# Kernel tuning notes

Hardware: AMD Instinct MI355X
Metric: run time of the kernel (lower is better)

Reference implementation:

```python
import jax, jax.numpy as jnp
import numpy as np

B, H, W = 8, 64, 64
DIM, NH, WS = 384, 6, 14
HD = DIM // NH
MLP = int(DIM * 4.0)
EPS = 1e-5
SCALE = HD ** -0.5


def setup_inputs() -> dict:
    key = jax.random.key(0)
    ks = jax.random.split(key, 8)
    init = lambda k, shape: (jax.random.normal(k, shape, dtype=jnp.float32) * 0.02)
    return {
        "x": jax.random.normal(ks[0], (B, H, W, DIM), dtype=jnp.float32),
        "ln1_w": jnp.ones((DIM,), jnp.float32),
        "ln1_b": jnp.zeros((DIM,), jnp.float32),
        "qkv_w": init(ks[1], (DIM, 3 * DIM)),
        "qkv_b": jnp.zeros((3 * DIM,), jnp.float32),
        "proj_w": init(ks[2], (DIM, DIM)),
        "proj_b": jnp.zeros((DIM,), jnp.float32),
        "rel_pos_h": init(ks[3], (2 * WS - 1, HD)),
        "rel_pos_w": init(ks[4], (2 * WS - 1, HD)),
        "ln2_w": jnp.ones((DIM,), jnp.float32),
        "ln2_b": jnp.zeros((DIM,), jnp.float32),
        "fc1_w": init(ks[5], (DIM, MLP)),
        "fc1_b": jnp.zeros((MLP,), jnp.float32),
        "fc2_w": init(ks[6], (MLP, DIM)),
        "fc2_b": jnp.zeros((DIM,), jnp.float32),
    }


def _layernorm(x, w, b):
    m = x.mean(-1, keepdims=True)
    v = ((x - m) ** 2).mean(-1, keepdims=True)
    return (x - m) * jax.lax.rsqrt(v + EPS) * w + b


def _get_rel_pos(rel_pos, ws):
    # q_size == k_size == ws and rel_pos has 2*ws-1 rows, so torch's
    # F.interpolate to max_rel_dist=2*ws-1 is an identity; direct indexing.
    coords = jnp.arange(ws)[:, None] - jnp.arange(ws)[None, :] + (ws - 1)
    return rel_pos[coords]  # (ws, ws, head_dim)


def _attention(xw, qkv_w, qkv_b, proj_w, proj_b, rel_pos_h, rel_pos_w):
    Bw = xw.shape[0]
    N = WS * WS
    qkv = xw.reshape(Bw, N, DIM) @ qkv_w + qkv_b  # (Bw, N, 3*DIM)
    qkv = qkv.reshape(Bw, N, 3, NH, HD).transpose(2, 0, 3, 1, 4).reshape(3, Bw * NH, N, HD)
    q, k, v = qkv[0], qkv[1], qkv[2]
    attn = jnp.einsum("bqd,bkd->bqk", q * SCALE, k)  # (Bw*NH, N, N)
    Rh = _get_rel_pos(rel_pos_h, WS)
    Rw = _get_rel_pos(rel_pos_w, WS)
    rq = q.reshape(Bw * NH, WS, WS, HD)
    rel_h = jnp.einsum("bhwc,hkc->bhwk", rq, Rh)
    rel_w = jnp.einsum("bhwc,wkc->bhwk", rq, Rw)
    attn = (attn.reshape(Bw * NH, WS, WS, WS, WS)
            + rel_h[:, :, :, :, None]
            + rel_w[:, :, :, None, :]).reshape(Bw * NH, N, N)
    attn = jax.nn.softmax(attn, axis=-1)
    out = jnp.einsum("bqk,bkd->bqd", attn, v)
    out = out.reshape(Bw, NH, WS, WS, HD).transpose(0, 2, 3, 1, 4).reshape(Bw, WS, WS, DIM)
    return out @ proj_w + proj_b


def reference(x, ln1_w, ln1_b, qkv_w, qkv_b, proj_w, proj_b, rel_pos_h, rel_pos_w,
              ln2_w, ln2_b, fc1_w, fc1_b, fc2_w, fc2_b):
    shortcut = x
    h = _layernorm(x, ln1_w, ln1_b)
    pad_h = (WS - H % WS) % WS
    pad_w = (WS - W % WS) % WS
    Hp, Wp = H + pad_h, W + pad_w
    hp = jnp.pad(h, ((0, 0), (0, pad_h), (0, pad_w), (0, 0)))
    # window partition: (B, Hp, Wp, C) -> (B*nWin, WS, WS, C)
    wins = hp.reshape(B, Hp // WS, WS, Wp // WS, WS, DIM)
    wins = wins.transpose(0, 1, 3, 2, 4, 5).reshape(-1, WS, WS, DIM)
    wins = _attention(wins, qkv_w, qkv_b, proj_w, proj_b, rel_pos_h, rel_pos_w)
    # window unpartition
    y = wins.reshape(B, Hp // WS, Wp // WS, WS, WS, DIM)
    y = y.transpose(0, 1, 3, 2, 4, 5).reshape(B, Hp, Wp, DIM)[:, :H, :W, :]
    x = shortcut + y
    h2 = _layernorm(x, ln2_w, ln2_b)
    mlp = jax.nn.gelu(h2 @ fc1_w + fc1_b, approximate=False) @ fc2_w + fc2_b
    return x + mlp
```

## Files before the change

### kernel.cpp

```cpp
#include <hip/hip_runtime.h>
#include <math.h>

#define DIMC 384
#define NHD  6
#define HD   64
#define WSZ  14
#define NTOK 196
#define NWIN 200
#define NWH  1200
#define MWIN 39200
#define MX   32768
#define MLPD 1536

typedef short short8 __attribute__((ext_vector_type(8)));
typedef float f32x4 __attribute__((ext_vector_type(4)));
typedef float f32x16 __attribute__((ext_vector_type(16)));

__device__ __forceinline__ unsigned short f2bf(float f) {
  unsigned int u = __float_as_uint(f);
  u = (u + 0x7fffu + ((u >> 16) & 1u)) >> 16;
  return (unsigned short)u;
}
__device__ __forceinline__ unsigned int pkbf(float a, float b) {
  unsigned int r; asm("v_cvt_pk_bf16_f32 %0, %1, %2" : "=v"(r) : "v"(a), "v"(b)); return r;
}
__device__ __forceinline__ float gelu_t(float x) {
  float z = 1.5957691216057308f * (x + 0.044715f * x * x * x);
  float e = __expf(z);
  float th = 1.f - 2.f * __builtin_amdgcn_rcpf(e + 1.f);
  return 0.5f * x * (1.f + th);
}

typedef const __attribute__((address_space(1))) unsigned int* gptr_t;
typedef __attribute__((address_space(3))) unsigned int* lptr_t;
__device__ __forceinline__ void gload16(const unsigned short* g, unsigned short* l) {
  __builtin_amdgcn_global_load_lds((gptr_t)(const void*)g, (lptr_t)(void*)l, 16, 0, 0);
}

__global__ void wtrans_kernel(const float* __restrict__ in, unsigned short* __restrict__ out,
                              int K, int N) {
  int id = blockIdx.x * 256 + threadIdx.x;
  if (id >= K * N) return;
  int n = id / K, k = id - n * K;
  out[id] = f2bf(in[(size_t)k * N + n]);
}

__global__ void relprep_kernel(const float* __restrict__ relh, const float* __restrict__ relw,
                               unsigned short* __restrict__ relcat) {
  int id = blockIdx.x * 256 + threadIdx.x;
  if (id >= 64 * 64) return;
  int rc = id >> 6, d = id & 63;
  float v = 0.f;
  if (rc < 27) v = relh[rc * 64 + d] * 8.f;
  else if (rc < 54) v = relw[(rc - 27) * 64 + d] * 8.f;
  relcat[id] = f2bf(v);
}

__global__ void vpad_kernel(unsigned short* __restrict__ vT) {
  int id = blockIdx.x * 256 + threadIdx.x;
  if (id >= 76800 * 3) return;
  int row = id / 3, part = id - row * 3;
  *(int2*)(vT + (size_t)row * 208 + 196 + part * 4) = make_int2(0, 0);
}

__global__ __launch_bounds__(64) void ln1win_kernel(const float* __restrict__ x,
    const float* __restrict__ w, const float* __restrict__ b, unsigned short* __restrict__ xw) {
  int t = blockIdx.x;
  int lane = threadIdx.x;
  int win = t / NTOK, p = t - win * NTOK;
  int bb = win / 25, rem = win - bb * 25;
  int wi = rem / 5, wj = rem - wi * 5;
  int i = p / WSZ, j = p - i * WSZ;
  int r = wi * WSZ + i, c = wj * WSZ + j;
  unsigned short* o = xw + (size_t)t * DIMC;
  if (r >= 64 || c >= 64) {
    #pragma unroll
    for (int q = 0; q < 6; q++) o[lane + q * 64] = 0;
    return;
  }
  const float* xr = x + (((size_t)bb * 64 + r) * 64 + c) * DIMC;
  float v[6]; float s = 0.f, s2 = 0.f;
  #pragma unroll
  for (int q = 0; q < 6; q++) { float f = xr[lane + q * 64]; v[q] = f; s += f; s2 += f * f; }
  #pragma unroll
  for (int off = 32; off; off >>= 1) { s += __shfl_xor(s, off); s2 += __shfl_xor(s2, off); }
  float mean = s * (1.f / DIMC);
  float var  = s2 * (1.f / DIMC) - mean * mean;
  float rstd = rsqrtf(var + 1e-5f);
  #pragma unroll
  for (int q = 0; q < 6; q++) {
    int d = lane + q * 64;
    o[d] = f2bf((v[q] - mean) * rstd * w[d] + b[d]);
  }
}

__global__ __launch_bounds__(64) void ln2_kernel(const float* __restrict__ x2,
    const float* __restrict__ w, const float* __restrict__ b, unsigned short* __restrict__ h2) {
  int t = blockIdx.x; int lane = threadIdx.x;
  const float* xr = x2 + (size_t)t * DIMC;
  unsigned short* o = h2 + (size_t)t * DIMC;
  float v[6]; float s = 0.f, s2 = 0.f;
  #pragma unroll
  for (int q = 0; q < 6; q++) { float f = xr[lane + q * 64]; v[q] = f; s += f; s2 += f * f; }
  #pragma unroll
  for (int off = 32; off; off >>= 1) { s += __shfl_xor(s, off); s2 += __shfl_xor(s2, off); }
  float mean = s * (1.f / DIMC);
  float var  = s2 * (1.f / DIMC) - mean * mean;
  float rstd = rsqrtf(var + 1e-5f);
  #pragma unroll
  for (int q = 0; q < 6; q++) {
    int d = lane + q * 64;
    o[d] = f2bf((v[q] - mean) * rstd * w[d] + b[d]);
  }
}

template <int EPI>
__global__ __launch_bounds__(256) void gemm_kernel(
    const unsigned short* __restrict__ A, const unsigned short* __restrict__ WT,
    int Mrows, int Kd,
    const float* __restrict__ bias, const float* __restrict__ addin,
    float* __restrict__ outf, unsigned short* __restrict__ outb,
    unsigned short* __restrict__ outb2) {
  __shared__ unsigned short As[3][128 * 32];
  __shared__ unsigned short Bs[3][128 * 32];
  const int nwg = gridDim.x * gridDim.y;
  const int flat = blockIdx.y * gridDim.x + blockIdx.x;
  const int xcd = flat & 7, q_ = nwg >> 3, r_ = nwg & 7;
  const int wg = (xcd < r_ ? xcd * (q_ + 1) : r_ * (q_ + 1) + (xcd - r_) * q_) + (flat >> 3);
  const int bx = wg / gridDim.y, by = wg - bx * gridDim.y;
  const int row0 = bx * 128, col0 = by * 128;
  const int tid = threadIdx.x;
  const int l = tid & 63, wid = tid >> 6;
  const int fr = l & 15, fk = (l >> 4) * 8;
  const int wr = (wid >> 1) * 64, wc = (wid & 1) * 64;
  const int sr = l >> 2, sc = (l & 3) * 8;
  const int scs = sc ^ (((sr >> 1) & 3) << 3);
  const int rsw = ((fr >> 1) & 3) << 3;
  f32x4 acc[4][4] = {};
  const unsigned short* ap = A + (size_t)row0 * Kd;
  const unsigned short* bp = WT + (size_t)col0 * Kd;
  const int nt = Kd >> 5;

  auto stage = [&](int t, int b) {
    const int k0 = t * 32;
    #pragma unroll
    for (int j = 0; j < 2; j++) {
      int chunk = j * 4 + wid;
      gload16(ap + (size_t)(chunk * 16 + sr) * Kd + k0 + scs, &As[b][chunk * 512]);
      gload16(bp + (size_t)(chunk * 16 + sr) * Kd + k0 + scs, &Bs[b][chunk * 512]);
    }
  };
  stage(0, 0);
  stage(1, 1);
  int c = 0;
  for (int t = 0; t < nt; ++t) {
    if (t < nt - 1) asm volatile("s_waitcnt vmcnt(4)" ::: "memory");
    else            asm volatile("s_waitcnt vmcnt(0)" ::: "memory");
    __builtin_amdgcn_s_barrier();
    __builtin_amdgcn_sched_barrier(0);
    if (t + 2 < nt) stage(t + 2, (c + 2 >= 3) ? c - 1 : c + 2);
    short8 a[4], b[4];
    #pragma unroll
    for (int fi = 0; fi < 4; fi++) {
      a[fi] = *(const short8*)&As[c][(wr + fi * 16 + fr) * 32 + (fk ^ rsw)];
      b[fi] = *(const short8*)&Bs[c][(wc + fi * 16 + fr) * 32 + (fk ^ rsw)];
    }
    asm volatile("s_waitcnt lgkmcnt(0)" ::: "memory");
    __builtin_amdgcn_sched_barrier(0);
    __builtin_amdgcn_s_setprio(1);
    #pragma unroll
    for (int fi = 0; fi < 4; fi++)
      #pragma unroll
      for (int fj = 0; fj < 4; fj++)
        acc[fi][fj] = __builtin_amdgcn_mfma_f32_16x16x32_bf16(b[fj], a[fi], acc[fi][fj], 0, 0, 0);
    __builtin_amdgcn_s_setprio(0);
    c = (c + 1 >= 3) ? 0 : c + 1;
  }
  #pragma unroll
  for (int fi = 0; fi < 4; fi++) {
    const int gr = row0 + wr + fi * 16 + fr;
    if (gr >= Mrows) continue;
    int wv_ = 0, p = 0, valid = 1; size_t pixbase = 0;
    if (EPI == 0 || EPI == 1) { wv_ = gr / NTOK; p = gr - wv_ * NTOK; }
    if (EPI == 1) {
      int bb = wv_ / 25, rem2 = wv_ - bb * 25;
      int wi = rem2 / 5, wj = rem2 - wi * 5;
      int i = p / WSZ, j = p - i * WSZ;
      int rr = wi * WSZ + i, cc = wj * WSZ + j;
      valid = (rr < 64) && (cc < 64);
      pixbase = (((size_t)bb * 64 + rr) * 64 + cc) * DIMC;
    }
    #pragma unroll
    for (int fj = 0; fj < 4; fj++) {
      const int gcb = col0 + wc + fj * 16 + (l >> 4) * 4;
      f32x4 v = acc[fi][fj];
      float4 bv = *(const float4*)&bias[gcb];
      float t0 = v[0] + bv.x, t1 = v[1] + bv.y, t2 = v[2] + bv.z, t3 = v[3] + bv.w;
      if (EPI == 0) {
        int s = gcb / 384, rem = gcb - s * 384;
        int hh = rem >> 6, d0 = gcb & 63;
        int whh = wv_ * NHD + hh;
        if (s == 0) { t0 *= 0.125f; t1 *= 0.125f; t2 *= 0.125f; t3 *= 0.125f; }
        if (s < 2) {
          *(int2*)&outb[((size_t)s * NWH + whh) * (NTOK * 64) + p * 64 + d0] =
              make_int2((int)pkbf(t0, t1), (int)pkbf(t2, t3));
        } else {
          unsigned short* vb = outb2 + ((size_t)whh * 64 + d0) * 208 + p;
          vb[0] = f2bf(t0); vb[208] = f2bf(t1); vb[416] = f2bf(t2); vb[624] = f2bf(t3);
        }
      } else if (EPI == 1) {
        if (valid) {
          size_t idx = pixbase + gcb;
          float4 ad = *(const float4*)&addin[idx];
          *(float4*)&outf[idx] = make_float4(t0 + ad.x, t1 + ad.y, t2 + ad.z, t3 + ad.w);
        }
      } else if (EPI == 2) {
        *(int2*)&outb[(size_t)gr * MLPD + gcb] =
            make_int2((int)pkbf(gelu_t(t0), gelu_t(t1)), (int)pkbf(gelu_t(t2), gelu_t(t3)));
      } else {
        size_t idx = (size_t)gr * DIMC + gcb;
        float4 ad = *(const float4*)&addin[idx];
        *(float4*)&outf[idx] = make_float4(t0 + ad.x, t1 + ad.y, t2 + ad.z, t3 + ad.w);
      }
    }
  }
}

template <bool TAIL>
__device__ __forceinline__ void attn_chunk(
    int kk, int l31, int hi,
    const unsigned short* __restrict__ kg,
    const unsigned short* __restrict__ VT,
    const short8* qf, const short8* qrel,
    f32x16& olo, f32x16& ohi_, float& m_reg, float& s_run) {
  int key = kk * 32 + l31;
  int keyc = (TAIL && key > 195) ? 195 : key;
  f32x16 S = {};
  __builtin_amdgcn_s_setprio(1);
  #pragma unroll
  for (int m = 0; m < 4; m++) {
    short8 kf = *(const short8*)(kg + (size_t)keyc * 64 + m * 16 + hi * 8);
    S = __builtin_amdgcn_mfma_f32_32x32x16_bf16(kf, qf[m], S, 0, 0, 0);
  }
  {
    int ki = keyc / 14, kj = keyc - ki * 14;
    #pragma unroll
    for (int m2 = 0; m2 < 2; m2++) {
      short8 kh;
      #pragma unroll
      for (int j = 0; j < 8; j++) {
        int cc = m2 * 16 + hi * 8 + j;
        kh[j] = (short)((cc == ki || cc == 14 + kj) ? 0x3F80 : 0);
      }
      S = __builtin_amdgcn_mfma_f32_32x32x16_bf16(kh, qrel[m2], S, 0, 0, 0);
    }
  }
  __builtin_amdgcn_s_setprio(0);
  float pmax = -3e38f;
  #pragma unroll
  for (int r = 0; r < 16; r++) {
    if (TAIL) {
      int krow = kk * 32 + (r & 3) + 8 * (r >> 2) + 4 * hi;
      if (krow >= 196) S[r] = -3e38f;
    }
    pmax = fmaxf(pmax, S[r]);
  }
  pmax = fmaxf(pmax, __shfl_xor(pmax, 32));
  if (__any(pmax > m_reg + 8.f)) {
    float m_new = fmaxf(m_reg, pmax);
    float fac = __expf(m_reg - m_new);
    m_reg = m_new;
    s_run *= fac;
    #pragma unroll
    for (int r = 0; r < 16; r++) {
      int qr = (r & 3) + 8 * (r >> 2) + 4 * hi;
      float fr_ = __shfl(fac, qr);
      olo[r] *= fr_; ohi_[r] *= fr_;
    }
  }
  float psum = 0.f;
  #pragma unroll
  for (int r = 0; r < 16; r++) { S[r] = __expf(S[r] - m_reg); psum += S[r]; }
  s_run += psum;
  unsigned int pk[8];
  #pragma unroll
  for (int t = 0; t < 8; t++) pk[t] = pkbf(S[2 * t], S[2 * t + 1]);
  #pragma unroll
  for (int m2 = 0; m2 < 2; m2++) {
    int b_ = m2 * 4;
    unsigned int x0 = (unsigned int)__shfl_xor((int)pk[b_ + 0], 32);
    unsigned int x1 = (unsigned int)__shfl_xor((int)pk[b_ + 1], 32);
    unsigned int x2 = (unsigned int)__shfl_xor((int)pk[b_ + 2], 32);
    unsigned int x3 = (unsigned int)__shfl_xor((int)pk[b_ + 3], 32);
    unsigned int au[4];
    au[0] = hi ? x2 : pk[b_ + 0];
    au[1] = hi ? x3 : pk[b_ + 1];
    au[2] = hi ? pk[b_ + 2] : x0;
    au[3] = hi ? pk[b_ + 3] : x1;
    short8 pa; __builtin_memcpy(&pa, au, 16);
    int kb = kk * 32 + m2 * 16 + hi * 8;
    if (TAIL && kb > 208) kb = 208;
    short8 vblo = *(const short8*)&VT[l31 * 216 + kb];
    short8 vbhi = *(const short8*)&VT[(32 + l31) * 216 + kb];
    __builtin_amdgcn_s_setprio(1);
    olo  = __builtin_amdgcn_mfma_f32_32x32x16_bf16(pa, vblo, olo, 0, 0, 0);
    ohi_ = __builtin_amdgcn_mfma_f32_32x32x16_bf16(pa, vbhi, ohi_, 0, 0, 0);
    __builtin_amdgcn_s_setprio(0);
  }
}

__global__ __launch_bounds__(256) void attn32_kernel(
    const unsigned short* __restrict__ qk_g,
    const unsigned short* __restrict__ vT_g,
    const unsigned short* __restrict__ relcat,
    unsigned short* __restrict__ attnout) {
  __shared__ __align__(16) unsigned short VT[64 * 216];
  __shared__ __align__(16) unsigned short RELB[4][2048];
  const int wh = blockIdx.x;
  const int w = wh / NHD, h = wh - w * NHD;
  const int tid = threadIdx.x;
  const unsigned short* vrow = vT_g + (size_t)wh * 64 * 208;
  for (int e = tid; e < 64 * 27; e += 256) {
    int d = e / 27, c = e - d * 27;
    int4 val = {0, 0, 0, 0};
    if (c < 26) val = *(const int4*)(vrow + d * 208 + c * 8);
    *(int4*)&VT[d * 216 + c * 8] = val;
  }
  __syncthreads();
  const int l = tid & 63, wv = tid >> 6;
  const int l31 = l & 31, hi = l >> 5;
  unsigned short* RB = &RELB[wv][0];
  const unsigned short* qg = qk_g + (size_t)wh * (NTOK * 64);
  const unsigned short* kg = qk_g + (size_t)(NWH + wh) * (NTOK * 64);

  for (int tile = wv; tile < 7; tile += 4) {
    const int q0 = tile * 32;
    int qrow = q0 + l31; if (qrow > 195) qrow = 195;
    short8 qf[4];
    #pragma unroll
    for (int m = 0; m < 4; m++)
      qf[m] = *(const short8*)(qg + (size_t)qrow * 64 + m * 16 + hi * 8);
    #pragma unroll
    for (int rt = 0; rt < 2; rt++) {
      f32x16 cr = {};
      __builtin_amdgcn_s_setprio(1);
      #pragma unroll
      for (int m = 0; m < 4; m++) {
        short8 af = *(const short8*)(relcat + (rt * 32 + l31) * 64 + m * 16 + hi * 8);
        cr = __builtin_amdgcn_mfma_f32_32x32x16_bf16(af, qf[m], cr, 0, 0, 0);
      }
      __builtin_amdgcn_s_setprio(0);
      #pragma unroll
      for (int t = 0; t < 8; t++) {
        int rr = rt * 32 + ((2 * t) & 3) + 8 * (t >> 1) + 4 * hi;
        *(unsigned int*)&RB[l31 * 64 + rr] = pkbf(cr[2 * t], cr[2 * t + 1]);
      }
    }
    __builtin_amdgcn_wave_barrier();
    int qi = qrow / 14, qj = qrow - qi * 14;
    short8 qrel[2];
    #pragma unroll
    for (int m2 = 0; m2 < 2; m2++)
      #pragma unroll
      for (int j = 0; j < 8; j++) {
        int cc = m2 * 16 + hi * 8 + j;
        unsigned short vv = 0;
        if (cc < 14) vv = RB[l31 * 64 + (qi - cc + 13)];
        else if (cc < 28) vv = RB[l31 * 64 + 27 + (qj - (cc - 14) + 13)];
        qrel[m2][j] = (short)vv;
      }
    __builtin_amdgcn_wave_barrier();
    f32x16 olo = {}, ohi_ = {};
    float m_reg = -3e38f, s_run = 0.f;
    for (int kk = 0; kk < 6; kk++)
      attn_chunk<false>(kk, l31, hi, kg, VT, qf, qrel, olo, ohi_, m_reg, s_run);
    attn_chunk<true>(6, l31, hi, kg, VT, qf, qrel, olo, ohi_, m_reg, s_run);
    s_run += __shfl_xor(s_run, 32);
    float inv = 1.f / s_run;
    #pragma unroll
    for (int r = 0; r < 16; r++) {
      int qr = (r & 3) + 8 * (r >> 2) + 4 * hi;
      float ir = __shfl(inv, qr);
      int tok = q0 + qr;
      if (tok < 196) {
        size_t base = ((size_t)w * NTOK + tok) * DIMC + h * 64;
        attnout[base + l31] = f2bf(olo[r] * ir);
        attnout[base + 32 + l31] = f2bf(ohi_[r] * ir);
      }
    }
  }
}

extern "C" void kernel_launch(void* const* d_in, const int* in_sizes, int n_in,
                              void* d_out, int out_size, void* d_ws, size_t ws_size,
                              hipStream_t stream) {
  const float* x     = (const float*)d_in[0];
  const float* ln1w  = (const float*)d_in[1];
  const float* ln1b  = (const float*)d_in[2];
  const float* qkvw  = (const float*)d_in[3];
  const float* qkvb  = (const float*)d_in[4];
  const float* projw = (const float*)d_in[5];
  const float* projb = (const float*)d_in[6];
  const float* relh  = (const float*)d_in[7];
  const float* relw  = (const float*)d_in[8];
  const float* ln2w  = (const float*)d_in[9];
  const float* ln2b  = (const float*)d_in[10];
  const float* fc1w  = (const float*)d_in[11];
  const float* fc1b  = (const float*)d_in[12];
  const float* fc2w  = (const float*)d_in[13];
  const float* fc2b  = (const float*)d_in[14];

  const size_t R0 = 0;
  const size_t R1 = R0 + 50331648;
  const size_t R2 = R1 + 100663296;
  const size_t R3 = R2 + 30105600;
  const size_t NEED = R3 + 3547136;
  if (ws_size < NEED) return;
  char* ws = (char*)d_ws;
  unsigned short* xw     = (unsigned short*)(ws + R0);
  float*          x2     = (float*)(ws + R0);
  unsigned short* qk_g   = (unsigned short*)(ws + R1);
  unsigned short* vT_g   = qk_g + (size_t)2 * NWH * NTOK * 64;
  unsigned short* hidden = (unsigned short*)(ws + R1);
  unsigned short* attno  = (unsigned short*)(ws + R2);
  unsigned short* h2     = (unsigned short*)(ws + R2);
  unsigned short* qkvwT  = (unsigned short*)(ws + R3);
  unsigned short* projwT = qkvwT + 442368;
  unsigned short* fc1wT  = projwT + 147456;
  unsigned short* fc2wT  = fc1wT + 589824;
  unsigned short* relcat = fc2wT + 589824;

  wtrans_kernel<<<1728, 256, 0, stream>>>(qkvw, qkvwT, 384, 1152);
  wtrans_kernel<<<576, 256, 0, stream>>>(projw, projwT, 384, 384);
  wtrans_kernel<<<2304, 256, 0, stream>>>(fc1w, fc1wT, 384, 1536);
  wtrans_kernel<<<2304, 256, 0, stream>>>(fc2w, fc2wT, 1536, 384);
  relprep_kernel<<<16, 256, 0, stream>>>(relh, relw, relcat);
  vpad_kernel<<<900, 256, 0, stream>>>(vT_g);
  ln1win_kernel<<<MWIN, 64, 0, stream>>>(x, ln1w, ln1b, xw);
  gemm_kernel<0><<<dim3(307, 9), 256, 0, stream>>>(xw, qkvwT, MWIN, 384, qkvb, nullptr, nullptr, qk_g, vT_g);
  attn32_kernel<<<NWH, 256, 0, stream>>>(qk_g, vT_g, relcat, attno);
  gemm_kernel<1><<<dim3(307, 3), 256, 0, stream>>>(attno, projwT, MWIN, 384, projb, x, x2, nullptr, nullptr);
  ln2_kernel<<<MX, 64, 0, stream>>>(x2, ln2w, ln2b, h2);
  gemm_kernel<2><<<dim3(256, 12), 256, 0, stream>>>(h2, fc1wT, MX, 384, fc1b, nullptr, nullptr, hidden, nullptr);
  gemm_kernel<3><<<dim3(256, 3), 256, 0, stream>>>(hidden, fc2wT, MX, 1536, fc2b, x2, (float*)d_out, nullptr, nullptr);
}
```

Measured before the change: 358.1 us.

## Enlarge GEMM tile to 256x128 and unroll triple-buffer pipeline by three

Doubles the GEMM row tile from 128 to 256, so each wave computes a 128x64 sub-tile with 8x4 MFMA accumulators. Arithmetic intensity per LDS and global load rises and grid sizes halve. The k-loop is unrolled by three with compile-time buffer indices, and the workspace is enlarged to cover over-read rows. This doubles accumulator registers and LDS use, which may lower occupancy, and leaves fewer workgroups to fill the CUs.

```diff
diff --git a/kernel.cpp b/kernel.cpp
--- a/kernel.cpp
+++ b/kernel.cpp
@@ -121,22 +121,22 @@
     const float* __restrict__ bias, const float* __restrict__ addin,
     float* __restrict__ outf, unsigned short* __restrict__ outb,
     unsigned short* __restrict__ outb2) {
-  __shared__ unsigned short As[3][128 * 32];
+  __shared__ unsigned short As[3][256 * 32];
   __shared__ unsigned short Bs[3][128 * 32];
   const int nwg = gridDim.x * gridDim.y;
   const int flat = blockIdx.y * gridDim.x + blockIdx.x;
   const int xcd = flat & 7, q_ = nwg >> 3, r_ = nwg & 7;
   const int wg = (xcd < r_ ? xcd * (q_ + 1) : r_ * (q_ + 1) + (xcd - r_) * q_) + (flat >> 3);
   const int bx = wg / gridDim.y, by = wg - bx * gridDim.y;
-  const int row0 = bx * 128, col0 = by * 128;
+  const int row0 = bx * 256, col0 = by * 128;
   const int tid = threadIdx.x;
   const int l = tid & 63, wid = tid >> 6;
   const int fr = l & 15, fk = (l >> 4) * 8;
-  const int wr = (wid >> 1) * 64, wc = (wid & 1) * 64;
+  const int wr = (wid >> 1) * 128, wc = (wid & 1) * 64;
   const int sr = l >> 2, sc = (l & 3) * 8;
   const int scs = sc ^ (((sr >> 1) & 3) << 3);
   const int rsw = ((fr >> 1) & 3) << 3;
-  f32x4 acc[4][4] = {};
+  f32x4 acc[8][4] = {};
   const unsigned short* ap = A + (size_t)row0 * Kd;
   const unsigned short* bp = WT + (size_t)col0 * Kd;
   const int nt = Kd >> 5;
@@ -144,40 +144,55 @@
   auto stage = [&](int t, int b) {
     const int k0 = t * 32;
     #pragma unroll
+    for (int j = 0; j < 4; j++) {
+      int chunk = j * 4 + wid;
+      gload16(ap + (size_t)(chunk * 16 + sr) * Kd + k0 + scs, &As[b][chunk * 512]);
+    }
+    #pragma unroll
     for (int j = 0; j < 2; j++) {
       int chunk = j * 4 + wid;
-      gload16(ap + (size_t)(chunk * 16 + sr) * Kd + k0 + scs, &As[b][chunk * 512]);
       gload16(bp + (size_t)(chunk * 16 + sr) * Kd + k0 + scs, &Bs[b][chunk * 512]);
     }
   };
   stage(0, 0);
   stage(1, 1);
-  int c = 0;
-  for (int t = 0; t < nt; ++t) {
-    if (t < nt - 1) asm volatile("s_waitcnt vmcnt(4)" ::: "memory");
-    else            asm volatile("s_waitcnt vmcnt(0)" ::: "memory");
-    __builtin_amdgcn_s_barrier();
-    __builtin_amdgcn_sched_barrier(0);
-    if (t + 2 < nt) stage(t + 2, (c + 2 >= 3) ? c - 1 : c + 2);
-    short8 a[4], b[4];
-    #pragma unroll
-    for (int fi = 0; fi < 4; fi++) {
-      a[fi] = *(const short8*)&As[c][(wr + fi * 16 + fr) * 32 + (fk ^ rsw)];
-      b[fi] = *(const short8*)&Bs[c][(wc + fi * 16 + fr) * 32 + (fk ^ rsw)];
-    }
-    asm volatile("s_waitcnt lgkmcnt(0)" ::: "memory");
-    __builtin_amdgcn_sched_barrier(0);
-    __builtin_amdgcn_s_setprio(1);
-    #pragma unroll
-    for (int fi = 0; fi < 4; fi++)
-      #pragma unroll
-      for (int fj = 0; fj < 4; fj++)
-        acc[fi][fj] = __builtin_amdgcn_mfma_f32_16x16x32_bf16(b[fj], a[fi], acc[fi][fj], 0, 0, 0);
-    __builtin_amdgcn_s_setprio(0);
-    c = (c + 1 >= 3) ? 0 : c + 1;
-  }
-  #pragma unroll
-  for (int fi = 0; fi < 4; fi++) {
+
+#define GSTEP(T, CB)                                                              \
+  {                                                                               \
+    const int t_ = (T);                                                           \
+    if (t_ < nt - 1) asm volatile("s_waitcnt vmcnt(6)" ::: "memory");             \
+    else             asm volatile("s_waitcnt vmcnt(0)" ::: "memory");             \
+    __builtin_amdgcn_s_barrier();                                                 \
+    __builtin_amdgcn_sched_barrier(0);                                            \
+    if (t_ + 2 < nt) stage(t_ + 2, ((CB) + 2) % 3);                               \
+    short8 a_[8], b_[4];                                                          \
+    _Pragma("unroll")                                                             \
+    for (int fi = 0; fi < 8; fi++)                                                \
+      a_[fi] = *(const short8*)&As[(CB)][(wr + fi * 16 + fr) * 32 + (fk ^ rsw)];  \
+    _Pragma("unroll")                                                             \
+    for (int fj = 0; fj < 4; fj++)                                                \
+      b_[fj] = *(const short8*)&Bs[(CB)][(wc + fj * 16 + fr) * 32 + (fk ^ rsw)];  \
+    asm volatile("s_waitcnt lgkmcnt(0)" ::: "memory");                            \
+    __builtin_amdgcn_sched_barrier(0);                                            \
+    __builtin_amdgcn_s_setprio(1);                                                \
+    _Pragma("unroll")                                                             \
+    for (int fi = 0; fi < 8; fi++)                                                \
+      _Pragma("unroll")                                                           \
+      for (int fj = 0; fj < 4; fj++)                                              \
+        acc[fi][fj] =                                                             \
+            __builtin_amdgcn_mfma_f32_16x16x32_bf16(b_[fj], a_[fi], acc[fi][fj], 0, 0, 0); \
+    __builtin_amdgcn_s_setprio(0);                                                \
+  }
+
+  for (int t = 0; t < nt; t += 3) {
+    GSTEP(t, 0)
+    GSTEP(t + 1, 1)
+    GSTEP(t + 2, 2)
+  }
+#undef GSTEP
+
+  #pragma unroll
+  for (int fi = 0; fi < 8; fi++) {
     const int gr = row0 + wr + fi * 16 + fr;
     if (gr >= Mrows) continue;
     int wv_ = 0, p = 0, valid = 1; size_t pixbase = 0;
@@ -413,7 +428,7 @@
   const size_t R0 = 0;
   const size_t R1 = R0 + 50331648;
   const size_t R2 = R1 + 100663296;
-  const size_t R3 = R2 + 30105600;
+  const size_t R3 = R2 + 30408704;
   const size_t NEED = R3 + 3547136;
   if (ws_size < NEED) return;
   char* ws = (char*)d_ws;
@@ -437,10 +452,10 @@
   relprep_kernel<<<16, 256, 0, stream>>>(relh, relw, relcat);
   vpad_kernel<<<900, 256, 0, stream>>>(vT_g);
   ln1win_kernel<<<MWIN, 64, 0, stream>>>(x, ln1w, ln1b, xw);
-  gemm_kernel<0><<<dim3(307, 9), 256, 0, stream>>>(xw, qkvwT, MWIN, 384, qkvb, nullptr, nullptr, qk_g, vT_g);
+  gemm_kernel<0><<<dim3(154, 9), 256, 0, stream>>>(xw, qkvwT, MWIN, 384, qkvb, nullptr, nullptr, qk_g, vT_g);
   attn32_kernel<<<NWH, 256, 0, stream>>>(qk_g, vT_g, relcat, attno);
-  gemm_kernel<1><<<dim3(307, 3), 256, 0, stream>>>(attno, projwT, MWIN, 384, projb, x, x2, nullptr, nullptr);
+  gemm_kernel<1><<<dim3(154, 3), 256, 0, stream>>>(attno, projwT, MWIN, 384, projb, x, x2, nullptr, nullptr);
   ln2_kernel<<<MX, 64, 0, stream>>>(x2, ln2w, ln2b, h2);
-  gemm_kernel<2><<<dim3(256, 12), 256, 0, stream>>>(h2, fc1wT, MX, 384, fc1b, nullptr, nullptr, hidden, nullptr);
-  gemm_kernel<3><<<dim3(256, 3), 256, 0, stream>>>(hidden, fc2wT, MX, 1536, fc2b, x2, (float*)d_out, nullptr, nullptr);
-}
+  gemm_kernel<2><<<dim3(128, 12), 256, 0, stream>>>(h2, fc1wT, MX, 384, fc1b, nullptr, nullptr, hidden, nullptr);
+  gemm_kernel<3><<<dim3(128, 3), 256, 0, stream>>>(hidden, fc2wT, MX, 1536, fc2b, x2, (float*)d_out, nullptr, nullptr);
+}
```

Result: slower. 505.4 us (+41.1%).
